# Kernel optimization log

Hardware: AMD Instinct MI355X
Metric: run time of the kernel (lower is better)

Reference implementation:

```python
import jax, jax.numpy as jnp
import numpy as np

T, B, H = 750, 1024, 100
TAU, DT, NOISE_STD = 0.01, 0.001, 0.1


def setup_inputs() -> dict:
    key = jax.random.key(0)
    ks = jax.random.split(key, 6)
    return {
        "input_seq": jax.random.normal(ks[0], (T, B, 4), jnp.float32),
        "noise": jax.random.normal(ks[1], (T, B, H), jnp.float32),
        "J_w": jax.random.normal(ks[2], (H, H), jnp.float32) * (H ** -0.5),
        "b_in": jax.random.normal(ks[3], (H, 4), jnp.float32) * 0.5,  # [b_m|b_c|b_cm|b_cc]
        "c_x": jnp.zeros((H,), jnp.float32),
        "wout_w": jax.random.normal(ks[4], (1, H), jnp.float32) * 0.01,
        "wout_b": jnp.zeros((1,), jnp.float32),
    }


def reference(input_seq, noise, J_w, b_in, c_x, wout_w, wout_b):
    alpha = DT / TAU  # dt/tau

    def step(x, ts):
        u, n = ts                      # u: [B,4], n: [B,H]
        r = jnp.tanh(x)
        input_term = u @ b_in.T        # [B,H] == sum_k u_k @ b_k.T
        dx = alpha * (-x + r @ J_w.T + input_term + c_x + NOISE_STD * n)
        x = x + dx
        return x, x

    x0 = jnp.zeros((input_seq.shape[1], H), input_seq.dtype)
    _, states = jax.lax.scan(step, x0, (input_seq, noise))  # states: [T,B,H]

    out_first = jnp.tanh(states[0]) @ wout_w.T + wout_b   # [B,1]
    out_final = jnp.tanh(states[-1]) @ wout_w.T + wout_b  # [B,1]
    outputs = jnp.stack([out_first[:, 0], out_final[:, 0]], axis=-1)  # [B,2]
    return outputs, states
```

## Files before the change

kernel.cpp:

```cpp
#include <hip/hip_runtime.h>


#define TSTEPS 750
#define BATCH  1024
#define HID    100
#define B_PER_BLK 4
#define THREADS (B_PER_BLK * HID)

constexpr float ALPHA = 0.1f;
constexpr float NSTD  = 0.1f;

__device__ __forceinline__ float ftanh(float x) {
    float e = __expf(2.0f * x);
    return 1.0f - 2.0f * __builtin_amdgcn_rcpf(e + 1.0f);
}

__global__ __launch_bounds__(THREADS) void rnn_scan_kernel(
    const float* __restrict__ input_seq,
    const float* __restrict__ noise,
    const float* __restrict__ J_w,
    const float* __restrict__ b_in,
    const float* __restrict__ c_x,
    float* __restrict__ states)
{
    const int tid = threadIdx.x;
    const int b_local = tid / HID;
    const int h = tid - b_local * HID;
    const int b = blockIdx.x * B_PER_BLK + b_local;

    float4 Jr[25];
    const float4* Jrow = reinterpret_cast<const float4*>(J_w + (size_t)h * HID);
#pragma unroll
    for (int i = 0; i < 25; ++i) Jr[i] = Jrow[i];

    const float4 bin = *reinterpret_cast<const float4*>(b_in + (size_t)h * 4);
    const float cx = c_x[h];

    __shared__ float r_lds[2][B_PER_BLK][HID];

    float x = 0.0f;
    r_lds[0][b_local][h] = 0.0f;

    const float* uptr = input_seq + (size_t)b * 4;
    const float* nptr = noise + (size_t)b * HID + h;
    float4 u  = *reinterpret_cast<const float4*>(uptr);
    float  nz = *nptr;

    float* sptr = states + (size_t)b * HID + h;

    __syncthreads();

    for (int t = 0; t < TSTEPS; ++t) {
        const int tn = (t + 1 < TSTEPS) ? (t + 1) : t;
        float4 u_next  = *reinterpret_cast<const float4*>(uptr + (size_t)tn * BATCH * 4);
        float  nz_next = nptr[(size_t)tn * BATCH * HID];

        const float* rb = &r_lds[t & 1][b_local][0];
        float a0 = 0.f, a1 = 0.f, a2 = 0.f, a3 = 0.f;
#pragma unroll
        for (int i = 0; i < 25; ++i) {
            float4 r4 = *reinterpret_cast<const float4*>(rb + 4 * i);
            a0 = fmaf(r4.x, Jr[i].x, a0);
            a1 = fmaf(r4.y, Jr[i].y, a1);
            a2 = fmaf(r4.z, Jr[i].z, a2);
            a3 = fmaf(r4.w, Jr[i].w, a3);
        }
        float s = (a0 + a1) + (a2 + a3);

        float inp = u.x * bin.x + u.y * bin.y + u.z * bin.z + u.w * bin.w;
        float dx = ALPHA * (-x + s + inp + cx + NSTD * nz);
        x += dx;

        sptr[(size_t)t * BATCH * HID] = x;
        r_lds[(t + 1) & 1][b_local][h] = ftanh(x);

        u = u_next; nz = nz_next;
        __syncthreads();
    }
}

__global__ __launch_bounds__(64) void rnn_out_kernel(
    const float* __restrict__ states,
    const float* __restrict__ wout_w,
    const float* __restrict__ wout_b,
    float* __restrict__ out)
{
    const int b = blockIdx.x;
    const int l = threadIdx.x;
    const float* s0 = states + (size_t)b * HID;
    const float* sF = states + ((size_t)(TSTEPS - 1) * BATCH + b) * HID;

    float p0 = 0.f, pF = 0.f;
    if (l < HID) {
        p0 = ftanh(s0[l]) * wout_w[l];
        pF = ftanh(sF[l]) * wout_w[l];
    }
    const int l2 = l + 64;
    if (l2 < HID) {
        p0 += ftanh(s0[l2]) * wout_w[l2];
        pF += ftanh(sF[l2]) * wout_w[l2];
    }
#pragma unroll
    for (int off = 32; off > 0; off >>= 1) {
        p0 += __shfl_xor(p0, off, 64);
        pF += __shfl_xor(pF, off, 64);
    }
    if (l == 0) {
        const float wb = wout_b[0];
        out[b * 2 + 0] = p0 + wb;
        out[b * 2 + 1] = pF + wb;
    }
}

extern "C" void kernel_launch(void* const* d_in, const int* in_sizes, int n_in,
                              void* d_out, int out_size, void* d_ws, size_t ws_size,
                              hipStream_t stream) {
    const float* input_seq = (const float*)d_in[0];
    const float* noise     = (const float*)d_in[1];
    const float* J_w       = (const float*)d_in[2];
    const float* b_in      = (const float*)d_in[3];
    const float* c_x       = (const float*)d_in[4];
    const float* wout_w    = (const float*)d_in[5];
    const float* wout_b    = (const float*)d_in[6];

    float* out    = (float*)d_out;
    float* states = out + 2 * BATCH;

    rnn_scan_kernel<<<BATCH / B_PER_BLK, THREADS, 0, stream>>>(
        input_seq, noise, J_w, b_in, c_x, states);
    rnn_out_kernel<<<BATCH, 64, 0, stream>>>(states, wout_w, wout_b, out);
}
```

Before: 546.0 us.

## Map one batch row per wavefront with packed FMA over hidden-unit pairs

The scan kernel now runs one 64-lane wavefront per batch element instead of four batch elements per 400-thread block. Fifty lanes each own two hidden units, hold the two matching J rows in registers as packed float pairs, and use packed FMAs for the recurrent matvec and the input projection. The block-wide __syncthreads between steps becomes a wave-level barrier, which removes the cross-wave synchronisation cost on the serial time loop. In exchange, 14 of 64 lanes sit idle, per-thread register use roughly doubles to hold 100 packed weights, and there is only one wave per block.

Result: slower. 683.6 us (+25.2%).

```diff
diff --git a/kernel.cpp b/kernel.cpp
--- a/kernel.cpp
+++ b/kernel.cpp
@@ -1,11 +1,11 @@
 #include <hip/hip_runtime.h>
 
+
+typedef float v2f __attribute__((ext_vector_type(2)));
 
 #define TSTEPS 750
 #define BATCH  1024
 #define HID    100
-#define B_PER_BLK 4
-#define THREADS (B_PER_BLK * HID)
 
 constexpr float ALPHA = 0.1f;
 constexpr float NSTD  = 0.1f;
@@ -15,7 +15,7 @@
     return 1.0f - 2.0f * __builtin_amdgcn_rcpf(e + 1.0f);
 }
 
-__global__ __launch_bounds__(THREADS) void rnn_scan_kernel(
+__global__ __launch_bounds__(64, 1) void rnn_scan_kernel(
     const float* __restrict__ input_seq,
     const float* __restrict__ noise,
     const float* __restrict__ J_w,
@@ -23,59 +23,78 @@
     const float* __restrict__ c_x,
     float* __restrict__ states)
 {
-    const int tid = threadIdx.x;
-    const int b_local = tid / HID;
-    const int h = tid - b_local * HID;
-    const int b = blockIdx.x * B_PER_BLK + b_local;
+    const int l = threadIdx.x;
+    const int b = blockIdx.x;
+    const bool act = (l < HID / 2);
+    const int le = act ? l : (HID / 2 - 1);
+    const int h0 = 2 * le;
 
-    float4 Jr[25];
-    const float4* Jrow = reinterpret_cast<const float4*>(J_w + (size_t)h * HID);
+    v2f Jp[HID];
+    const float4* rA = reinterpret_cast<const float4*>(J_w + (size_t)h0 * HID);
 #pragma unroll
-    for (int i = 0; i < 25; ++i) Jr[i] = Jrow[i];
+    for (int i = 0; i < 25; ++i) {
+        float4 a = rA[i];
+        float4 c = rA[i + 25];
+        Jp[4*i+0] = (v2f){a.x, c.x};
+        Jp[4*i+1] = (v2f){a.y, c.y};
+        Jp[4*i+2] = (v2f){a.z, c.z};
+        Jp[4*i+3] = (v2f){a.w, c.w};
+    }
+    float4 ba = reinterpret_cast<const float4*>(b_in)[h0];
+    float4 bc = reinterpret_cast<const float4*>(b_in)[h0 + 1];
+    v2f binp0 = (v2f){ba.x, bc.x}, binp1 = (v2f){ba.y, bc.y};
+    v2f binp2 = (v2f){ba.z, bc.z}, binp3 = (v2f){ba.w, bc.w};
+    v2f cxp = (v2f){c_x[h0], c_x[h0 + 1]};
 
-    const float4 bin = *reinterpret_cast<const float4*>(b_in + (size_t)h * 4);
-    const float cx = c_x[h];
+    __shared__ __align__(16) float rbuf[2][HID];
 
-    __shared__ float r_lds[2][B_PER_BLK][HID];
+    v2f x = (v2f){0.f, 0.f};
+    if (act) *reinterpret_cast<v2f*>(&rbuf[0][h0]) = (v2f){0.f, 0.f};
+    __builtin_amdgcn_wave_barrier();
 
-    float x = 0.0f;
-    r_lds[0][b_local][h] = 0.0f;
+    const float* np = noise + (size_t)b * HID + h0;
+    const float* up = input_seq + (size_t)b * 4;
+    float* sp = states + (size_t)b * HID + h0;
 
-    const float* uptr = input_seq + (size_t)b * 4;
-    const float* nptr = noise + (size_t)b * HID + h;
-    float4 u  = *reinterpret_cast<const float4*>(uptr);
-    float  nz = *nptr;
-
-    float* sptr = states + (size_t)b * HID + h;
-
-    __syncthreads();
+    v2f   nz = *reinterpret_cast<const v2f*>(np);
+    float4 u = *reinterpret_cast<const float4*>(up);
 
     for (int t = 0; t < TSTEPS; ++t) {
         const int tn = (t + 1 < TSTEPS) ? (t + 1) : t;
-        float4 u_next  = *reinterpret_cast<const float4*>(uptr + (size_t)tn * BATCH * 4);
-        float  nz_next = nptr[(size_t)tn * BATCH * HID];
+        v2f   nz_n = *reinterpret_cast<const v2f*>(np + (size_t)tn * BATCH * HID);
+        float4 u_n = *reinterpret_cast<const float4*>(up + (size_t)tn * BATCH * 4);
 
-        const float* rb = &r_lds[t & 1][b_local][0];
-        float a0 = 0.f, a1 = 0.f, a2 = 0.f, a3 = 0.f;
+        const float* rb = rbuf[t & 1];
+        v2f a0 = {0,0}, a1 = {0,0}, a2 = {0,0}, a3 = {0,0};
 #pragma unroll
         for (int i = 0; i < 25; ++i) {
             float4 r4 = *reinterpret_cast<const float4*>(rb + 4 * i);
-            a0 = fmaf(r4.x, Jr[i].x, a0);
-            a1 = fmaf(r4.y, Jr[i].y, a1);
-            a2 = fmaf(r4.z, Jr[i].z, a2);
-            a3 = fmaf(r4.w, Jr[i].w, a3);
+            a0 = __builtin_elementwise_fma(Jp[4*i+0], (v2f){r4.x, r4.x}, a0);
+            a1 = __builtin_elementwise_fma(Jp[4*i+1], (v2f){r4.y, r4.y}, a1);
+            a2 = __builtin_elementwise_fma(Jp[4*i+2], (v2f){r4.z, r4.z}, a2);
+            a3 = __builtin_elementwise_fma(Jp[4*i+3], (v2f){r4.w, r4.w}, a3);
         }
-        float s = (a0 + a1) + (a2 + a3);
+        a0 = __builtin_elementwise_fma(binp0, (v2f){u.x, u.x}, a0);
+        a1 = __builtin_elementwise_fma(binp1, (v2f){u.y, u.y}, a1);
+        a2 = __builtin_elementwise_fma(binp2, (v2f){u.z, u.z}, a2);
+        a3 = __builtin_elementwise_fma(binp3, (v2f){u.w, u.w}, a3);
+        v2f s = (a0 + a1) + (a2 + a3);
 
-        float inp = u.x * bin.x + u.y * bin.y + u.z * bin.z + u.w * bin.w;
-        float dx = ALPHA * (-x + s + inp + cx + NSTD * nz);
-        x += dx;
+        v2f pre = s + cxp;
+        pre = __builtin_elementwise_fma((v2f){NSTD, NSTD}, nz, pre);
+        x = __builtin_elementwise_fma((v2f){ALPHA, ALPHA}, pre - x, x);
 
-        sptr[(size_t)t * BATCH * HID] = x;
-        r_lds[(t + 1) & 1][b_local][h] = ftanh(x);
+        v2f r;
+        r.x = ftanh(x.x);
+        r.y = ftanh(x.y);
 
-        u = u_next; nz = nz_next;
-        __syncthreads();
+        if (act) {
+            *reinterpret_cast<v2f*>(sp + (size_t)t * BATCH * HID) = x;
+            *reinterpret_cast<v2f*>(&rbuf[(t + 1) & 1][h0]) = r;
+        }
+        __builtin_amdgcn_wave_barrier();
+        nz = nz_n;
+        u  = u_n;
     }
 }
 
@@ -126,7 +145,7 @@
     float* out    = (float*)d_out;
     float* states = out + 2 * BATCH;
 
-    rnn_scan_kernel<<<BATCH / B_PER_BLK, THREADS, 0, stream>>>(
+    rnn_scan_kernel<<<BATCH, 64, 0, stream>>>(
         input_seq, noise, J_w, b_in, c_x, states);
     rnn_out_kernel<<<BATCH, 64, 0, stream>>>(states, wout_w, wout_b, out);
 }
```

## Compute recurrent matvec with bf16 split-precision MFMA over 16-row batch tiles

Applied to the files above, without the earlier changes.

Replaces the per-thread FP32 dot-product recurrence with 16x16x32 bf16 MFMA instructions. Each block now handles 16 batch rows with 7 waves covering the hidden dimension. Weights and tanh activations are split into hi/lo bf16 pairs, and three MFMAs approximate FP32 accuracy. This removes most scalar FMA and LDS float4 traffic per step. In exchange it drops the software prefetch of the next step's noise and inputs, uses a hand-placed barrier, and carries some precision risk from the bf16 three-term approximation.

After: 955.4 us. 1.75x slower.

```diff
diff --git a/kernel.cpp b/kernel.cpp
--- a/kernel.cpp
+++ b/kernel.cpp
@@ -1,11 +1,17 @@
 #include <hip/hip_runtime.h>
+#include <hip/hip_bf16.h>
 
+
+typedef __attribute__((ext_vector_type(8))) short bf16x8;
+typedef __attribute__((ext_vector_type(4))) float f32x4;
 
 #define TSTEPS 750
 #define BATCH  1024
 #define HID    100
-#define B_PER_BLK 4
-#define THREADS (B_PER_BLK * HID)
+#define NT     7
+#define KT     4
+#define KSTRIDE 136
+#define THREADS (NT * 64)
 
 constexpr float ALPHA = 0.1f;
 constexpr float NSTD  = 0.1f;
@@ -15,67 +21,119 @@
     return 1.0f - 2.0f * __builtin_amdgcn_rcpf(e + 1.0f);
 }
 
-__global__ __launch_bounds__(THREADS) void rnn_scan_kernel(
-    const float* __restrict__ input_seq,
-    const float* __restrict__ noise,
-    const float* __restrict__ J_w,
-    const float* __restrict__ b_in,
-    const float* __restrict__ c_x,
-    float* __restrict__ states)
+__device__ __forceinline__ void bsplit(float v, unsigned& hi, unsigned& lo) {
+    __hip_bfloat16 h = __float2bfloat16(v);
+    unsigned hb = *reinterpret_cast<unsigned short*>(&h);
+    float hf = __builtin_bit_cast(float, hb << 16);
+    __hip_bfloat16 l = __float2bfloat16(v - hf);
+    hi = hb;
+    lo = *reinterpret_cast<unsigned short*>(&l);
+}
+
+__global__ void __launch_bounds__(THREADS)
+__attribute__((amdgpu_waves_per_eu(1, 2)))
+rnn_mfma_kernel(const float* __restrict__ input_seq,
+                const float* __restrict__ noise,
+                const float* __restrict__ J_w,
+                const float* __restrict__ b_in,
+                const float* __restrict__ c_x,
+                float* __restrict__ states)
 {
     const int tid = threadIdx.x;
-    const int b_local = tid / HID;
-    const int h = tid - b_local * HID;
-    const int b = blockIdx.x * B_PER_BLK + b_local;
+    const int w   = tid >> 6;
+    const int l   = tid & 63;
+    const int lr  = l & 15;
+    const int lg  = l >> 4;
+    const int bid = blockIdx.x;
 
-    float4 Jr[25];
-    const float4* Jrow = reinterpret_cast<const float4*>(J_w + (size_t)h * HID);
+    const int  h    = w * 16 + lr;
+    const bool hval = (h < HID);
+    const int  hc   = hval ? h : (HID - 1);
+
+    __shared__ __align__(16) unsigned short rHI[2][16][KSTRIDE];
+    __shared__ __align__(16) unsigned short rLO[2][16][KSTRIDE];
+
+    for (int i = tid; i < 2 * 16 * KSTRIDE; i += THREADS) {
+        (&rHI[0][0][0])[i] = 0;
+        (&rLO[0][0][0])[i] = 0;
+    }
+
+    int4 BH[KT], BL[KT];
 #pragma unroll
-    for (int i = 0; i < 25; ++i) Jr[i] = Jrow[i];
+    for (int t = 0; t < KT; ++t) {
+        unsigned hs[8], ls[8];
+#pragma unroll
+        for (int j = 0; j < 8; ++j) {
+            int k = 32 * t + 8 * lg + j;
+            float v = (hval && k < HID) ? J_w[(size_t)hc * HID + k] : 0.0f;
+            bsplit(v, hs[j], ls[j]);
+        }
+        BH[t] = make_int4((int)(hs[0] | (hs[1] << 16)), (int)(hs[2] | (hs[3] << 16)),
+                          (int)(hs[4] | (hs[5] << 16)), (int)(hs[6] | (hs[7] << 16)));
+        BL[t] = make_int4((int)(ls[0] | (ls[1] << 16)), (int)(ls[2] | (ls[3] << 16)),
+                          (int)(ls[4] | (ls[5] << 16)), (int)(ls[6] | (ls[7] << 16)));
+    }
+#define PINV(q) asm volatile("" : "+v"(q.x), "+v"(q.y), "+v"(q.z), "+v"(q.w));
+    PINV(BH[0]) PINV(BH[1]) PINV(BH[2]) PINV(BH[3])
+    PINV(BL[0]) PINV(BL[1]) PINV(BL[2]) PINV(BL[3])
+#undef PINV
 
-    const float4 bin = *reinterpret_cast<const float4*>(b_in + (size_t)h * 4);
-    const float cx = c_x[h];
+    const float4 binp = *reinterpret_cast<const float4*>(b_in + (size_t)hc * 4);
+    const float  cx   = c_x[hc];
 
-    __shared__ float r_lds[2][B_PER_BLK][HID];
+    float x0 = 0.f, x1 = 0.f, x2 = 0.f, x3 = 0.f;
 
-    float x = 0.0f;
-    r_lds[0][b_local][h] = 0.0f;
-
-    const float* uptr = input_seq + (size_t)b * 4;
-    const float* nptr = noise + (size_t)b * HID + h;
-    float4 u  = *reinterpret_cast<const float4*>(uptr);
-    float  nz = *nptr;
-
-    float* sptr = states + (size_t)b * HID + h;
+    const size_t bbase = (size_t)bid * 16;
 
     __syncthreads();
 
     for (int t = 0; t < TSTEPS; ++t) {
-        const int tn = (t + 1 < TSTEPS) ? (t + 1) : t;
-        float4 u_next  = *reinterpret_cast<const float4*>(uptr + (size_t)tn * BATCH * 4);
-        float  nz_next = nptr[(size_t)tn * BATCH * HID];
+        const int cur = t & 1, nxt = cur ^ 1;
 
-        const float* rb = &r_lds[t & 1][b_local][0];
-        float a0 = 0.f, a1 = 0.f, a2 = 0.f, a3 = 0.f;
+        float nz[4], ud[4];
 #pragma unroll
-        for (int i = 0; i < 25; ++i) {
-            float4 r4 = *reinterpret_cast<const float4*>(rb + 4 * i);
-            a0 = fmaf(r4.x, Jr[i].x, a0);
-            a1 = fmaf(r4.y, Jr[i].y, a1);
-            a2 = fmaf(r4.z, Jr[i].z, a2);
-            a3 = fmaf(r4.w, Jr[i].w, a3);
+        for (int i = 0; i < 4; ++i) {
+            const size_t b_i = bbase + 4 * lg + i;
+            nz[i] = noise[((size_t)t * BATCH + b_i) * HID + hc];
+            float4 uu = *reinterpret_cast<const float4*>(input_seq + ((size_t)t * BATCH + b_i) * 4);
+            ud[i] = uu.x * binp.x + uu.y * binp.y + uu.z * binp.z + uu.w * binp.w;
         }
-        float s = (a0 + a1) + (a2 + a3);
 
-        float inp = u.x * bin.x + u.y * bin.y + u.z * bin.z + u.w * bin.w;
-        float dx = ALPHA * (-x + s + inp + cx + NSTD * nz);
-        x += dx;
+        f32x4 aA = {0.f, 0.f, 0.f, 0.f}, aB = aA, aC = aA;
+#pragma unroll
+        for (int kt = 0; kt < KT; ++kt) {
+            const int eoff = (4 * kt + lg) * 8;
+            bf16x8 ah = *reinterpret_cast<const bf16x8*>(&rHI[cur][lr][eoff]);
+            bf16x8 al = *reinterpret_cast<const bf16x8*>(&rLO[cur][lr][eoff]);
+            bf16x8 jh = __builtin_bit_cast(bf16x8, BH[kt]);
+            bf16x8 jl = __builtin_bit_cast(bf16x8, BL[kt]);
+            aA = __builtin_amdgcn_mfma_f32_16x16x32_bf16(ah, jh, aA, 0, 0, 0);
+            aB = __builtin_amdgcn_mfma_f32_16x16x32_bf16(al, jh, aB, 0, 0, 0);
+            aC = __builtin_amdgcn_mfma_f32_16x16x32_bf16(ah, jl, aC, 0, 0, 0);
+        }
+        f32x4 dot = (aA + aB) + aC;
 
-        sptr[(size_t)t * BATCH * HID] = x;
-        r_lds[(t + 1) & 1][b_local][h] = ftanh(x);
+        float xs[4] = {x0, x1, x2, x3};
+#pragma unroll
+        for (int i = 0; i < 4; ++i) {
+            float pre = dot[i] + ud[i] + cx + NSTD * nz[i];
+            float xn = xs[i] + ALPHA * (pre - xs[i]);
+            xs[i] = xn;
+            const size_t b_i = bbase + 4 * lg + i;
+            if (hval) {
+                states[((size_t)t * BATCH + b_i) * HID + h] = xn;
+                unsigned rh, rl;
+                bsplit(ftanh(xn), rh, rl);
+                const int m = 4 * lg + i;
+                rHI[nxt][m][h] = (unsigned short)rh;
+                rLO[nxt][m][h] = (unsigned short)rl;
+            }
+        }
+        x0 = xs[0]; x1 = xs[1]; x2 = xs[2]; x3 = xs[3];
 
-        u = u_next; nz = nz_next;
-        __syncthreads();
+        asm volatile("s_waitcnt lgkmcnt(0)" ::: "memory");
+        __builtin_amdgcn_s_barrier();
+        __builtin_amdgcn_sched_barrier(0);
     }
 }
 
@@ -126,7 +184,7 @@
     float* out    = (float*)d_out;
     float* states = out + 2 * BATCH;
 
-    rnn_scan_kernel<<<BATCH / B_PER_BLK, THREADS, 0, stream>>>(
+    rnn_mfma_kernel<<<BATCH / 16, THREADS, 0, stream>>>(
         input_seq, noise, J_w, b_in, c_x, states);
     rnn_out_kernel<<<BATCH, 64, 0, stream>>>(states, wout_w, wout_b, out);
 }
```
